# Performance work log

Hardware: AMD Instinct MI355X
Metric: run time of the kernel (lower is better)

## Reference

```python
import jax, jax.numpy as jnp
import numpy as np

DIM = 512
DEPTH = 6
HEADS = 8
HD = DIM // HEADS          # head dim = 64
HALF = HD // 4             # rope half_dim = 16
MLP_H = int(DIM * 4.0)
TOKENS = [1, 4, 16, 64]    # CLS, S1, S2, S3
N = sum(TOKENS)            # 85
MAX_FREQ = 10.0
BATCH = 1024
LN_EPS = 1e-5


def _build_mask():
    # CLS sees CLS+S3; each scale sees CLS+itself (block-diagonal + CLS column)
    m = np.full((N, N), -np.inf, dtype=np.float32)
    cum = np.cumsum([0] + TOKENS)  # [0,1,5,21,85]
    m[0, 0] = 0.0
    m[0, cum[3]:cum[4]] = 0.0
    for i in range(1, 4):
        s, e = cum[i], cum[i + 1]
        m[s:e, 0] = 0.0
        m[s:e, s:e] = 0.0
    return jnp.asarray(m)

MASK = _build_mask()
FREQS = jnp.exp(jnp.arange(HALF, dtype=jnp.float32) * (-np.log(MAX_FREQ) / HALF))


def _layer_norm(x, g, b):
    mu = x.mean(-1, keepdims=True)
    var = ((x - mu) ** 2).mean(-1, keepdims=True)
    return (x - mu) * jax.lax.rsqrt(var + LN_EPS) * g + b


def _rope2d(t, coords):
    # t: [B,H,P,HD], coords: [P,2] in [0,1]^2
    ang_x = coords[:, 0:1] * FREQS[None, :] * (2.0 * jnp.pi)  # [P,HALF]
    ang_y = coords[:, 1:2] * FREQS[None, :] * (2.0 * jnp.pi)
    cx, sx = jnp.cos(ang_x), jnp.sin(ang_x)
    cy, sy = jnp.cos(ang_y), jnp.sin(ang_y)
    B, H, P, _ = t.shape
    t = t.reshape(B, H, P, 4, HALF)
    x0, x1, x2, x3 = t[..., 0, :], t[..., 1, :], t[..., 2, :], t[..., 3, :]
    r = jnp.stack([x0 * cx - x1 * sx,
                   x0 * sx + x1 * cx,
                   x2 * cy - x3 * sy,
                   x2 * sy + x3 * cy], axis=3)
    return r.reshape(B, H, P, HD)


def _rope_skip_cls(t, coords):
    return jnp.concatenate([t[:, :, :1], _rope2d(t[:, :, 1:], coords)], axis=2)


def _block(x, coords, p):
    (ln1g, ln1b, qkvw, qkvb, projw, projb,
     ln2g, ln2b, f1w, f1b, f2w, f2b) = p
    B, Nn, D = x.shape
    h = _layer_norm(x, ln1g, ln1b)
    qkv = h @ qkvw + qkvb                         # [B,N,3D]
    qkv = qkv.reshape(B, Nn, 3, HEADS, HD).transpose(2, 0, 3, 1, 4)
    q, k, v = qkv[0], qkv[1], qkv[2]              # [B,H,N,HD]
    q = _rope_skip_cls(q, coords)
    k = _rope_skip_cls(k, coords)
    attn = jnp.einsum('bhqd,bhkd->bhqk', q, k) * (HD ** -0.5) + MASK
    attn = jax.nn.softmax(attn, axis=-1)
    out = jnp.einsum('bhqk,bhkd->bhqd', attn, v)
    out = out.transpose(0, 2, 1, 3).reshape(B, Nn, D)
    x = x + (out @ projw + projb)
    h = _layer_norm(x, ln2g, ln2b)
    h = jax.nn.gelu(h @ f1w + f1b, approximate=False) @ f2w + f2b
    return x + h


def setup_inputs() -> dict:
    key = jax.random.key(0)
    ks = jax.random.split(key, 8)
    s = 0.02
    nrm = lambda k, shape: jax.random.normal(k, shape, jnp.float32) * s
    return dict(
        x=jax.random.normal(ks[0], (BATCH, N, DIM), jnp.float32),
        coords=jax.random.uniform(ks[1], (N - 1, 2), jnp.float32),
        ln1_g=jnp.ones((DEPTH, DIM), jnp.float32),
        ln1_b=jnp.zeros((DEPTH, DIM), jnp.float32),
        qkv_w=nrm(ks[2], (DEPTH, DIM, 3 * DIM)),
        qkv_b=jnp.zeros((DEPTH, 3 * DIM), jnp.float32),
        proj_w=nrm(ks[3], (DEPTH, DIM, DIM)),
        proj_b=jnp.zeros((DEPTH, DIM), jnp.float32),
        ln2_g=jnp.ones((DEPTH, DIM), jnp.float32),
        ln2_b=jnp.zeros((DEPTH, DIM), jnp.float32),
        fc1_w=nrm(ks[4], (DEPTH, DIM, MLP_H)),
        fc1_b=jnp.zeros((DEPTH, MLP_H), jnp.float32),
        fc2_w=nrm(ks[5], (DEPTH, MLP_H, DIM)),
        fc2_b=jnp.zeros((DEPTH, DIM), jnp.float32),
    )


def reference(x, coords, ln1_g, ln1_b, qkv_w, qkv_b, proj_w, proj_b,
              ln2_g, ln2_b, fc1_w, fc1_b, fc2_w, fc2_b):
    for i in range(DEPTH):
        x = _block(x, coords,
                   (ln1_g[i], ln1_b[i], qkv_w[i], qkv_b[i], proj_w[i], proj_b[i],
                    ln2_g[i], ln2_b[i], fc1_w[i], fc1_b[i], fc2_w[i], fc2_b[i]))
    return x
```

## Files before the change

kernel.cpp:

```cpp
#include <hip/hip_runtime.h>
#include <hip/hip_bf16.h>
#include <math.h>

#define DIMX 512
#define NTOK 85
#define BATCH 1024
#define M_ROWS (BATCH * NTOK)
#define MLP_H 2048
#define DEPTH 6

typedef __attribute__((ext_vector_type(8))) short short8;
typedef __attribute__((ext_vector_type(4))) float f32x4;

__device__ inline float bf2f(ushort u) {
    union { unsigned int i; float f; } v; v.i = ((unsigned int)u) << 16; return v.f;
}
__device__ inline ushort f2bf(float f) {
    __hip_bfloat16 h = __float2bfloat16(f);
    union { __hip_bfloat16 h; ushort u; } v; v.h = h; return v.u;
}
__device__ inline unsigned int pack2(float a, float b) {
    return (unsigned int)f2bf(a) | ((unsigned int)f2bf(b) << 16);
}
__device__ inline float gelu_fast(float v) {
    float u = 1.5957691f * fmaf(0.044715f * v, v * v, v);
    return v / (1.0f + __expf(-u));
}

__device__ inline void gload16(const ushort* g, ushort* lds) {
    __builtin_amdgcn_global_load_lds(
        (const __attribute__((address_space(1))) unsigned int*)g,
        (__attribute__((address_space(3))) unsigned int*)lds, 16, 0, 0);
}

__global__ __launch_bounds__(256) void transpose_bf16(const float* __restrict__ in,
                                                      ushort* __restrict__ out,
                                                      int K, int N) {
    __shared__ float tile[32][33];
    int n0 = blockIdx.x * 32, k0 = blockIdx.y * 32;
    int tx = threadIdx.x, ty = threadIdx.y;
    #pragma unroll
    for (int j = 0; j < 32; j += 8)
        tile[ty + j][tx] = in[(size_t)(k0 + ty + j) * N + n0 + tx];
    __syncthreads();
    #pragma unroll
    for (int j = 0; j < 32; j += 8)
        out[(size_t)(n0 + ty + j) * K + k0 + tx] = f2bf(tile[tx][ty + j]);
}

__global__ void rope_table(const float* __restrict__ coords, float* __restrict__ tab) {
    int t = blockIdx.x;
    int idx = threadIdx.x;
    float freq = expf(-(float)idx * (2.302585093f / 16.0f));
    float twopi = 6.283185307179586f;
    float ax = coords[t * 2 + 0] * freq * twopi;
    float ay = coords[t * 2 + 1] * freq * twopi;
    tab[t * 64 + idx]      = cosf(ax);
    tab[t * 64 + 16 + idx] = sinf(ax);
    tab[t * 64 + 32 + idx] = cosf(ay);
    tab[t * 64 + 48 + idx] = sinf(ay);
}

__global__ __launch_bounds__(256) void ln_kernel(const float* __restrict__ x,
                                                 const float* __restrict__ g,
                                                 const float* __restrict__ bta,
                                                 ushort* __restrict__ out) {
    int w = threadIdx.x >> 6, lane = threadIdx.x & 63;
    size_t row = (size_t)blockIdx.x * 4 + w;
    const float* xr = x + row * DIMX;
    int c = lane * 8;
    float4 v0 = *(const float4*)(xr + c);
    float4 v1 = *(const float4*)(xr + c + 4);
    float s = v0.x + v0.y + v0.z + v0.w + v1.x + v1.y + v1.z + v1.w;
    #pragma unroll
    for (int m = 32; m; m >>= 1) s += __shfl_xor(s, m);
    float mu = s * (1.0f / 512.0f);
    float d0 = v0.x - mu, d1 = v0.y - mu, d2 = v0.z - mu, d3 = v0.w - mu;
    float d4 = v1.x - mu, d5 = v1.y - mu, d6 = v1.z - mu, d7 = v1.w - mu;
    float q = d0*d0 + d1*d1 + d2*d2 + d3*d3 + d4*d4 + d5*d5 + d6*d6 + d7*d7;
    #pragma unroll
    for (int m = 32; m; m >>= 1) q += __shfl_xor(q, m);
    float rs = rsqrtf(q * (1.0f / 512.0f) + 1e-5f);
    float4 g0 = *(const float4*)(g + c), g1 = *(const float4*)(g + c + 4);
    float4 b0 = *(const float4*)(bta + c), b1 = *(const float4*)(bta + c + 4);
    uint4 o;
    o.x = pack2(d0 * rs * g0.x + b0.x, d1 * rs * g0.y + b0.y);
    o.y = pack2(d2 * rs * g0.z + b0.z, d3 * rs * g0.w + b0.w);
    o.z = pack2(d4 * rs * g1.x + b1.x, d5 * rs * g1.y + b1.y);
    o.w = pack2(d6 * rs * g1.z + b1.z, d7 * rs * g1.w + b1.w);
    *(uint4*)&out[row * DIMX + c] = o;
}

template <int EPI>
__global__ __launch_bounds__(256, 2) void gemm_wide(const ushort* __restrict__ A,
                                                    const ushort* __restrict__ Bt,
                                                    const float* __restrict__ bias,
                                                    const float* __restrict__ inF,
                                                    float* __restrict__ outF,
                                                    ushort* __restrict__ outB,
                                                    int M, int N, int K,
                                                    const float* __restrict__ tab) {
    __shared__ ushort AsF[3 * 8192] __attribute__((aligned(16)));
    __shared__ ushort BsF[3 * 4096] __attribute__((aligned(16)));
    int tid = threadIdx.x;
    int w = tid >> 6, lane = tid & 63;
    int wm2 = (w >> 1) * 128;
    int wn = (w & 1) * 64;

    int nbx = gridDim.x;
    int nwg = nbx * gridDim.y;
    int orig = blockIdx.y * nbx + blockIdx.x;
    int q8 = nwg >> 3, r8 = nwg & 7;
    int xcd = orig & 7, loc = orig >> 3;
    int id = (xcd < r8) ? xcd * (q8 + 1) + loc : r8 * (q8 + 1) + (xcd - r8) * q8 + loc;
    int m0 = (id / nbx) * 256;
    int n0 = (id % nbx) * 128;

    int srow = tid >> 2;
    int scol = ((tid & 3) ^ ((srow >> 1) & 3)) * 8;
    int rA0 = m0 + srow;       if (rA0 >= M) rA0 = M - 1;
    int rA1 = m0 + 64 + srow;  if (rA1 >= M) rA1 = M - 1;
    int rA2 = m0 + 128 + srow; if (rA2 >= M) rA2 = M - 1;
    int rA3 = m0 + 192 + srow; if (rA3 >= M) rA3 = M - 1;
    const ushort* gA0 = A + (size_t)rA0 * K + scol;
    const ushort* gA1 = A + (size_t)rA1 * K + scol;
    const ushort* gA2 = A + (size_t)rA2 * K + scol;
    const ushort* gA3 = A + (size_t)rA3 * K + scol;
    const ushort* gB0 = Bt + (size_t)(n0 + srow) * K + scol;
    const ushort* gB1 = Bt + (size_t)(n0 + 64 + srow) * K + scol;
    int dwz = w * 512;
    int swA = 0, swB = 0;

#define STAGEW() do {                                                          \
        gload16(gA0, &AsF[swA + dwz]);                                         \
        gload16(gA1, &AsF[swA + 2048 + dwz]);                                  \
        gload16(gA2, &AsF[swA + 4096 + dwz]);                                  \
        gload16(gA3, &AsF[swA + 6144 + dwz]);                                  \
        gload16(gB0, &BsF[swB + dwz]);                                         \
        gload16(gB1, &BsF[swB + 2048 + dwz]);                                  \
        gA0 += 32; gA1 += 32; gA2 += 32; gA3 += 32; gB0 += 32; gB1 += 32;      \
        swA += 8192; if (swA == 24576) swA = 0;                                \
        swB += 4096; if (swB == 12288) swB = 0; } while (0)

    int l15 = lane & 15, lq = lane >> 4;
    int sw = (lq ^ ((l15 >> 1) & 3)) * 8;
    int aoff = (wm2 + l15) * 32 + sw;
    int boff = (wn + l15) * 32 + sw;
    int roffA = 0, roffB = 0;

    int NT = K >> 5;
    STAGEW(); STAGEW();

    f32x4 acc[8][4] = {};

    for (int t = 0; t < NT; ++t) {
        if (t < NT - 1) asm volatile("s_waitcnt vmcnt(6)" ::: "memory");
        else            asm volatile("s_waitcnt vmcnt(0)" ::: "memory");
        __builtin_amdgcn_s_barrier();
        short8 a[8], b[4];
        #pragma unroll
        for (int i = 0; i < 8; i++) a[i] = *(const short8*)&AsF[roffA + aoff + i * 512];
        #pragma unroll
        for (int j = 0; j < 4; j++) b[j] = *(const short8*)&BsF[roffB + boff + j * 512];
        if (t + 2 < NT) STAGEW();
        __builtin_amdgcn_s_setprio(1);
        #pragma unroll
        for (int i = 0; i < 8; i++)
            #pragma unroll
            for (int j = 0; j < 4; j++)
                acc[i][j] = __builtin_amdgcn_mfma_f32_16x16x32_bf16(a[i], b[j], acc[i][j], 0, 0, 0);
        __builtin_amdgcn_s_setprio(0);
        roffA += 8192; if (roffA == 24576) roffA = 0;
        roffB += 4096; if (roffB == 12288) roffB = 0;
    }
#undef STAGEW

    int cr = lq * 4;
    int cc = l15;
    if (EPI == 0) {
        bool ropeReg = (n0 + wn) < 1024;
        int gnb = n0 + wn + cc;
        float bb0 = bias[gnb], bb1 = bias[gnb + 16], bb2 = bias[gnb + 32], bb3 = bias[gnb + 48];
        #pragma unroll
        for (int i = 0; i < 8; i++) {
            #pragma unroll
            for (int rr = 0; rr < 4; rr++) {
                int gm = m0 + wm2 + i * 16 + cr + rr;
                if (gm >= M) continue;
                int n = gm % NTOK;
                float v0 = acc[i][0][rr] + bb0;
                float v1 = acc[i][1][rr] + bb1;
                float v2 = acc[i][2][rr] + bb2;
                float v3 = acc[i][3][rr] + bb3;
                if (ropeReg && n > 0) {
                    const float* tt = tab + (size_t)(n - 1) * 64 + cc;
                    float cx = tt[0], sx = tt[16], cy = tt[32], sy = tt[48];
                    float y0 = v0 * cx - v1 * sx;
                    float y1 = v0 * sx + v1 * cx;
                    float y2 = v2 * cy - v3 * sy;
                    float y3 = v2 * sy + v3 * cy;
                    v0 = y0; v1 = y1; v2 = y2; v3 = y3;
                }
                size_t o = (size_t)gm * N + gnb;
                outB[o]      = f2bf(v0);
                outB[o + 16] = f2bf(v1);
                outB[o + 32] = f2bf(v2);
                outB[o + 48] = f2bf(v3);
            }
        }
    } else {
        #pragma unroll
        for (int i = 0; i < 8; i++) {
            #pragma unroll
            for (int rr = 0; rr < 4; rr++) {
                int gm = m0 + wm2 + i * 16 + cr + rr;
                if (gm >= M) continue;
                #pragma unroll
                for (int j = 0; j < 4; j++) {
                    int gn = n0 + wn + j * 16 + cc;
                    float v = acc[i][j][rr] + bias[gn];
                    size_t o = (size_t)gm * N + gn;
                    if (EPI == 1) {
                        outF[o] = inF[o] + v;
                    } else {
                        outB[o] = f2bf(gelu_fast(v));
                    }
                }
            }
        }
    }
}

__global__ __launch_bounds__(256, 2) void gemm_nb(const ushort* __restrict__ A,
                                                  const ushort* __restrict__ Bt,
                                                  const float* __restrict__ bias,
                                                  ushort* __restrict__ outB,
                                                  int M, int N, int K) {
    __shared__ ushort LDS[4 * 10240] __attribute__((aligned(16)));
    int tid = threadIdx.x;
    int w = tid >> 6, lane = tid & 63;
    int wm = (w >> 1) * 96;
    int wn = (w & 1) * 64;

    int nbx = gridDim.x;
    int nwg = nbx * gridDim.y;
    int orig = blockIdx.y * nbx + blockIdx.x;
    int q8 = nwg >> 3, r8 = nwg & 7;
    int xcd = orig & 7, loc = orig >> 3;
    int id = (xcd < r8) ? xcd * (q8 + 1) + loc : r8 * (q8 + 1) + (xcd - r8) * q8 + loc;
    int m0 = (id / nbx) * 192;
    int n0 = (id % nbx) * 128;

    int srow = lane >> 2;
    int scol = ((lane & 3) ^ ((srow >> 1) & 3)) * 8;
    const ushort* pA[6];
    const ushort* pB[4];
    #pragma unroll
    for (int i = 0; i < 6; i++) {
        int r = m0 + wm + i * 16 + srow; if (r >= M) r = M - 1;
        pA[i] = A + (size_t)r * K + scol;
    }
    #pragma unroll
    for (int j = 0; j < 4; j++)
        pB[j] = Bt + (size_t)(n0 + wn + j * 16 + srow) * K + scol;

    ushort* LW = &LDS[w * 10240];

#define STAGE_NB(T) do { int kc = (T) * 32, s = ((T) & 1);                     \
        int da = s * 3072, db = 6144 + s * 2048;                               \
        gload16(pA[0] + kc, &LW[da]);                                          \
        gload16(pA[1] + kc, &LW[da + 512]);                                    \
        gload16(pA[2] + kc, &LW[da + 1024]);                                   \
        gload16(pA[3] + kc, &LW[da + 1536]);                                   \
        gload16(pA[4] + kc, &LW[da + 2048]);                                   \
        gload16(pA[5] + kc, &LW[da + 2560]);                                   \
        gload16(pB[0] + kc, &LW[db]);                                          \
        gload16(pB[1] + kc, &LW[db + 512]);                                    \
        gload16(pB[2] + kc, &LW[db + 1024]);                                   \
        gload16(pB[3] + kc, &LW[db + 1536]); } while (0)

    int l15 = lane & 15, lq = lane >> 4;
    int sw = (lq ^ ((l15 >> 1) & 3)) * 8;
    int foff = l15 * 32 + sw;

    int NT = K >> 5;
    STAGE_NB(0);

    f32x4 acc[6][4] = {};

    for (int t = 0; t < NT; ++t) {
        int ra = (t & 1) * 3072, rb = 6144 + (t & 1) * 2048;
        if (t + 1 < NT) {
            asm volatile("s_waitcnt lgkmcnt(0)" ::: "memory");
            STAGE_NB(t + 1);
            asm volatile("s_waitcnt vmcnt(10)" ::: "memory");
        } else {
            asm volatile("s_waitcnt vmcnt(0)" ::: "memory");
        }
        short8 a[6], b[4];
        #pragma unroll
        for (int i = 0; i < 6; i++) a[i] = *(const short8*)&LW[ra + foff + i * 512];
        #pragma unroll
        for (int j = 0; j < 4; j++) b[j] = *(const short8*)&LW[rb + foff + j * 512];
        __builtin_amdgcn_s_setprio(1);
        #pragma unroll
        for (int i = 0; i < 6; i++)
            #pragma unroll
            for (int j = 0; j < 4; j++)
                acc[i][j] = __builtin_amdgcn_mfma_f32_16x16x32_bf16(a[i], b[j], acc[i][j], 0, 0, 0);
        __builtin_amdgcn_s_setprio(0);
    }
#undef STAGE_NB

    int cr = lq * 4;
    int cc = l15;
    #pragma unroll
    for (int i = 0; i < 6; i++) {
        #pragma unroll
        for (int rr = 0; rr < 4; rr++) {
            int gm = m0 + wm + i * 16 + cr + rr;
            if (gm >= M) continue;
            #pragma unroll
            for (int j = 0; j < 4; j++) {
                int gn = n0 + wn + j * 16 + cc;
                float v = acc[i][j][rr] + bias[gn];
                outB[(size_t)gm * N + gn] = f2bf(gelu_fast(v));
            }
        }
    }
}

__global__ __launch_bounds__(384) void attn_kernel(const ushort* __restrict__ qkv,
                                                   ushort* __restrict__ out) {
    __shared__ ushort SU[13824] __attribute__((aligned(16)));
    __shared__ ushort Vt[6656]  __attribute__((aligned(16)));
    int bh = blockIdx.x;
    int b = bh >> 3, h = bh & 7;
    int tid = threadIdx.x;
    size_t base = (size_t)b * NTOK * 1536 + h * 64;

    for (int it = tid; it < 1536; it += 384) {
        int mat = (it >= 768) ? 1 : 0;
        int item = it - mat * 768;
        int n = item >> 3, g = item & 7;
        short8 v = {};
        if (n < NTOK)
            v = *(const short8*)&qkv[base + (size_t)n * 1536 + mat * 512 + g * 8];
        *(short8*)&SU[mat * 6912 + n * 72 + g * 8] = v;
    }
    for (int it = tid; it < 768; it += 384) {
        int n = it % 96;
        int d0 = (it / 96) * 8;
        short8 v = {};
        if (n < NTOK)
            v = *(const short8*)&qkv[base + (size_t)n * 1536 + 1024 + d0];
        #pragma unroll
        for (int j = 0; j < 8; j++)
            Vt[(d0 + j) * 104 + n] = (ushort)v[j];
    }
    __syncthreads();

    int wid = tid >> 6;
    int lane = tid & 63;
    int q = lane >> 4, c = lane & 15;
    int i0 = wid * 16;

    f32x4 acc[6] = {};
    #pragma unroll
    for (int kk = 0; kk < 2; kk++) {
        short8 aq = *(const short8*)&SU[(i0 + c) * 72 + kk * 32 + q * 8];
        #pragma unroll
        for (int t = 0; t < 6; t++) {
            short8 bk = *(const short8*)&SU[6912 + (t * 16 + c) * 72 + kk * 32 + q * 8];
            acc[t] = __builtin_amdgcn_mfma_f32_16x16x32_bf16(aq, bk, acc[t], 0, 0, 0);
        }
    }
    __syncthreads();

    #pragma unroll
    for (int r = 0; r < 4; r++) {
        int i = i0 + q * 4 + r;
        int si = (i == 0) ? 3 : (i < 5 ? 1 : (i < 21 ? 2 : 3));
        float vs[6];
        float m = -1e30f;
        #pragma unroll
        for (int t = 0; t < 6; t++) {
            int j = t * 16 + c;
            int sj = (j == 0) ? si : (j < 5 ? 1 : (j < 21 ? 2 : (j < NTOK ? 3 : -1)));
            float v = (sj == si) ? acc[t][r] * 0.125f : -1e30f;
            vs[t] = v;
            m = fmaxf(m, v);
        }
        #pragma unroll
        for (int mk = 8; mk; mk >>= 1) m = fmaxf(m, __shfl_xor(m, mk));
        float s = 0.f, ps[6];
        #pragma unroll
        for (int t = 0; t < 6; t++) { ps[t] = __expf(vs[t] - m); s += ps[t]; }
        #pragma unroll
        for (int mk = 8; mk; mk >>= 1) s += __shfl_xor(s, mk);
        float inv = 1.0f / s;
        #pragma unroll
        for (int t = 0; t < 6; t++)
            SU[i * 104 + t * 16 + c] = f2bf(ps[t] * inv);
    }
    __syncthreads();

    f32x4 o2[4] = {};
    #pragma unroll
    for (int kk = 0; kk < 3; kk++) {
        short8 ap = *(const short8*)&SU[(i0 + c) * 104 + kk * 32 + q * 8];
        #pragma unroll
        for (int nt = 0; nt < 4; nt++) {
            short8 bv = *(const short8*)&Vt[(nt * 16 + c) * 104 + kk * 32 + q * 8];
            o2[nt] = __builtin_amdgcn_mfma_f32_16x16x32_bf16(ap, bv, o2[nt], 0, 0, 0);
        }
    }
    size_t orow = (size_t)b * NTOK;
    #pragma unroll
    for (int nt = 0; nt < 4; nt++) {
        #pragma unroll
        for (int r = 0; r < 4; r++) {
            int i = i0 + q * 4 + r;
            if (i < NTOK)
                out[(orow + i) * DIMX + h * 64 + nt * 16 + c] = f2bf(o2[nt][r]);
        }
    }
}

extern "C" void kernel_launch(void* const* d_in, const int* in_sizes, int n_in,
                              void* d_out, int out_size, void* d_ws, size_t ws_size,
                              hipStream_t stream) {
    const float* x_in    = (const float*)d_in[0];
    const float* coords  = (const float*)d_in[1];
    const float* ln1_g   = (const float*)d_in[2];
    const float* ln1_b   = (const float*)d_in[3];
    const float* qkv_w   = (const float*)d_in[4];
    const float* qkv_b   = (const float*)d_in[5];
    const float* proj_w  = (const float*)d_in[6];
    const float* proj_b  = (const float*)d_in[7];
    const float* ln2_g   = (const float*)d_in[8];
    const float* ln2_b   = (const float*)d_in[9];
    const float* fc1_w   = (const float*)d_in[10];
    const float* fc1_b   = (const float*)d_in[11];
    const float* fc2_w   = (const float*)d_in[12];
    const float* fc2_b   = (const float*)d_in[13];

    char* ws = (char*)d_ws;
    size_t off = 0;
    auto alloc = [&](size_t bytes) -> void* {
        void* p = ws + off;
        off += (bytes + 255) & ~(size_t)255;
        return p;
    };
    auto asz = [](size_t b) { return (b + 255) & ~(size_t)255; };

    const size_t WPL = 512 * 1536 + 512 * 512 + 512 * 2048 + 2048 * 512;

    size_t fixed = asz(WPL * DEPTH * sizeof(ushort)) + asz(84 * 64 * sizeof(float));
    int Bc = 1024;
    while (Bc > 4) {
        size_t rc = (size_t)Bc * NTOK;
        size_t need = fixed + asz(rc * DIMX * sizeof(ushort)) + asz(rc * MLP_H * sizeof(ushort));
        if (need <= ws_size) break;
        Bc >>= 1;
    }
    size_t Rc = (size_t)Bc * NTOK;

    ushort* wt   = (ushort*)alloc(WPL * DEPTH * sizeof(ushort));
    float*  tab  = (float*)alloc(84 * 64 * sizeof(float));
    ushort* hbuf = (ushort*)alloc(Rc * DIMX * sizeof(ushort));
    ushort* big  = (ushort*)alloc(Rc * MLP_H * sizeof(ushort));

    rope_table<<<84, 16, 0, stream>>>(coords, tab);

    dim3 tb(32, 8);
    for (int l = 0; l < DEPTH; l++) {
        ushort* wl = wt + (size_t)l * WPL;
        transpose_bf16<<<dim3(1536 / 32, 512 / 32), tb, 0, stream>>>(
            qkv_w + (size_t)l * 512 * 1536, wl, 512, 1536);
        transpose_bf16<<<dim3(512 / 32, 512 / 32), tb, 0, stream>>>(
            proj_w + (size_t)l * 512 * 512, wl + 786432, 512, 512);
        transpose_bf16<<<dim3(2048 / 32, 512 / 32), tb, 0, stream>>>(
            fc1_w + (size_t)l * 512 * 2048, wl + 1048576, 512, 2048);
        transpose_bf16<<<dim3(512 / 32, 2048 / 32), tb, 0, stream>>>(
            fc2_w + (size_t)l * 2048 * 512, wl + 2097152, 2048, 512);
    }

    int mt256 = (int)(Rc / 256);
    int mt192 = (int)((Rc + 191) / 192);
    int lnblocks = (int)(Rc / 4);
    for (int c = 0; c < BATCH / Bc; c++) {
        float* xc = (float*)d_out + (size_t)c * Rc * DIMX;
        const float* xin_c = x_in + (size_t)c * Rc * DIMX;
        int Mc = (int)Rc;
        for (int l = 0; l < DEPTH; l++) {
            ushort* wl = wt + (size_t)l * WPL;
            const float* xsrc = (l == 0) ? xin_c : xc;
            ln_kernel<<<lnblocks, 256, 0, stream>>>(
                xsrc, ln1_g + l * 512, ln1_b + l * 512, hbuf);
            gemm_wide<0><<<dim3(1536 / 128, mt256), 256, 0, stream>>>(
                hbuf, wl, qkv_b + (size_t)l * 1536, nullptr, nullptr, big,
                Mc, 1536, 512, tab);
            attn_kernel<<<Bc * 8, 384, 0, stream>>>(big, hbuf);
            gemm_wide<1><<<dim3(512 / 128, mt256), 256, 0, stream>>>(
                hbuf, wl + 786432, proj_b + (size_t)l * 512, xsrc, xc, nullptr,
                Mc, 512, 512, nullptr);
            ln_kernel<<<lnblocks, 256, 0, stream>>>(
                xc, ln2_g + l * 512, ln2_b + l * 512, hbuf);
            gemm_nb<<<dim3(2048 / 128, mt192), 256, 0, stream>>>(
                hbuf, wl + 1048576, fc1_b + (size_t)l * 2048, big,
                Mc, 2048, 512);
            gemm_wide<1><<<dim3(512 / 128, mt256), 256, 0, stream>>>(
                big, wl + 2097152, fc2_b + (size_t)l * 512, xc, xc, nullptr,
                Mc, 512, 2048, nullptr);
        }
    }
}
```

Measured before the change: 7.209 ms.

## Replace per-wave fc1 GEMM with shared-LDS 512-thread triple-buffered kernel

The fc1 GEMM moves from a 256-thread kernel, where each wave staged its own private A/B tiles (192x128 block), to a 512-thread kernel with a 256x128 block tile. The eight waves share A/B tiles in LDS through a three-stage ring buffer with barrier synchronisation. This removes redundant global loads of shared operand rows and gives deeper prefetch. It adds block-wide barriers, fewer accumulators per wave, and a templated epilogue that also carries an unused RoPE path for the qkv GEMM.

```diff
diff --git a/kernel.cpp b/kernel.cpp
--- a/kernel.cpp
+++ b/kernel.cpp
@@ -231,15 +231,20 @@
     }
 }
 
-__global__ __launch_bounds__(256, 2) void gemm_nb(const ushort* __restrict__ A,
-                                                  const ushort* __restrict__ Bt,
-                                                  const float* __restrict__ bias,
-                                                  ushort* __restrict__ outB,
-                                                  int M, int N, int K) {
-    __shared__ ushort LDS[4 * 10240] __attribute__((aligned(16)));
+template <int EPI>
+__global__ __launch_bounds__(512, 4) void gemm_e(const ushort* __restrict__ A,
+                                                 const ushort* __restrict__ Bt,
+                                                 const float* __restrict__ bias,
+                                                 const float* __restrict__ inF,
+                                                 float* __restrict__ outF,
+                                                 ushort* __restrict__ outB,
+                                                 int M, int N, int K,
+                                                 const float* __restrict__ tab) {
+    __shared__ ushort AsF[3 * 8192] __attribute__((aligned(16)));
+    __shared__ ushort BsF[3 * 4096] __attribute__((aligned(16)));
     int tid = threadIdx.x;
     int w = tid >> 6, lane = tid & 63;
-    int wm = (w >> 1) * 96;
+    int wm = (w >> 1) * 64;
     int wn = (w & 1) * 64;
 
     int nbx = gridDim.x;
@@ -248,83 +253,111 @@
     int q8 = nwg >> 3, r8 = nwg & 7;
     int xcd = orig & 7, loc = orig >> 3;
     int id = (xcd < r8) ? xcd * (q8 + 1) + loc : r8 * (q8 + 1) + (xcd - r8) * q8 + loc;
-    int m0 = (id / nbx) * 192;
+    int m0 = (id / nbx) * 256;
     int n0 = (id % nbx) * 128;
 
-    int srow = lane >> 2;
-    int scol = ((lane & 3) ^ ((srow >> 1) & 3)) * 8;
-    const ushort* pA[6];
-    const ushort* pB[4];
-    #pragma unroll
-    for (int i = 0; i < 6; i++) {
-        int r = m0 + wm + i * 16 + srow; if (r >= M) r = M - 1;
-        pA[i] = A + (size_t)r * K + scol;
-    }
-    #pragma unroll
-    for (int j = 0; j < 4; j++)
-        pB[j] = Bt + (size_t)(n0 + wn + j * 16 + srow) * K + scol;
-
-    ushort* LW = &LDS[w * 10240];
-
-#define STAGE_NB(T) do { int kc = (T) * 32, s = ((T) & 1);                     \
-        int da = s * 3072, db = 6144 + s * 2048;                               \
-        gload16(pA[0] + kc, &LW[da]);                                          \
-        gload16(pA[1] + kc, &LW[da + 512]);                                    \
-        gload16(pA[2] + kc, &LW[da + 1024]);                                   \
-        gload16(pA[3] + kc, &LW[da + 1536]);                                   \
-        gload16(pA[4] + kc, &LW[da + 2048]);                                   \
-        gload16(pA[5] + kc, &LW[da + 2560]);                                   \
-        gload16(pB[0] + kc, &LW[db]);                                          \
-        gload16(pB[1] + kc, &LW[db + 512]);                                    \
-        gload16(pB[2] + kc, &LW[db + 1024]);                                   \
-        gload16(pB[3] + kc, &LW[db + 1536]); } while (0)
+    int srow = tid >> 2;
+    int scol = ((tid & 3) ^ ((srow >> 1) & 3)) * 8;
+    int rA0 = m0 + srow;        if (rA0 >= M) rA0 = M - 1;
+    int rA1 = m0 + 128 + srow;  if (rA1 >= M) rA1 = M - 1;
+    const ushort* gA0 = A + (size_t)rA0 * K + scol;
+    const ushort* gA1 = A + (size_t)rA1 * K + scol;
+    const ushort* gB0 = Bt + (size_t)(n0 + srow) * K + scol;
+    int dwz = w * 512;
+    int swA = 0, swB = 0;
+
+#define STAGEE() do {                                                          \
+        gload16(gA0, &AsF[swA + dwz]);                                         \
+        gload16(gA1, &AsF[swA + 4096 + dwz]);                                  \
+        gload16(gB0, &BsF[swB + dwz]);                                         \
+        gA0 += 32; gA1 += 32; gB0 += 32;                                       \
+        swA += 8192; if (swA == 24576) swA = 0;                                \
+        swB += 4096; if (swB == 12288) swB = 0; } while (0)
 
     int l15 = lane & 15, lq = lane >> 4;
     int sw = (lq ^ ((l15 >> 1) & 3)) * 8;
-    int foff = l15 * 32 + sw;
+    int aoff = (wm + l15) * 32 + sw;
+    int boff = (wn + l15) * 32 + sw;
+    int roffA = 0, roffB = 0;
 
     int NT = K >> 5;
-    STAGE_NB(0);
-
-    f32x4 acc[6][4] = {};
+    STAGEE(); STAGEE();
+
+    f32x4 acc[4][4] = {};
 
     for (int t = 0; t < NT; ++t) {
-        int ra = (t & 1) * 3072, rb = 6144 + (t & 1) * 2048;
-        if (t + 1 < NT) {
-            asm volatile("s_waitcnt lgkmcnt(0)" ::: "memory");
-            STAGE_NB(t + 1);
-            asm volatile("s_waitcnt vmcnt(10)" ::: "memory");
-        } else {
-            asm volatile("s_waitcnt vmcnt(0)" ::: "memory");
-        }
-        short8 a[6], b[4];
-        #pragma unroll
-        for (int i = 0; i < 6; i++) a[i] = *(const short8*)&LW[ra + foff + i * 512];
-        #pragma unroll
-        for (int j = 0; j < 4; j++) b[j] = *(const short8*)&LW[rb + foff + j * 512];
+        if (t < NT - 1) asm volatile("s_waitcnt vmcnt(3)" ::: "memory");
+        else            asm volatile("s_waitcnt vmcnt(0)" ::: "memory");
+        __builtin_amdgcn_s_barrier();
+        short8 a[4], b[4];
+        #pragma unroll
+        for (int i = 0; i < 4; i++) a[i] = *(const short8*)&AsF[roffA + aoff + i * 512];
+        #pragma unroll
+        for (int j = 0; j < 4; j++) b[j] = *(const short8*)&BsF[roffB + boff + j * 512];
+        if (t + 2 < NT) STAGEE();
         __builtin_amdgcn_s_setprio(1);
         #pragma unroll
-        for (int i = 0; i < 6; i++)
+        for (int i = 0; i < 4; i++)
             #pragma unroll
             for (int j = 0; j < 4; j++)
                 acc[i][j] = __builtin_amdgcn_mfma_f32_16x16x32_bf16(a[i], b[j], acc[i][j], 0, 0, 0);
         __builtin_amdgcn_s_setprio(0);
-    }
-#undef STAGE_NB
+        roffA += 8192; if (roffA == 24576) roffA = 0;
+        roffB += 4096; if (roffB == 12288) roffB = 0;
+    }
+#undef STAGEE
 
     int cr = lq * 4;
     int cc = l15;
-    #pragma unroll
-    for (int i = 0; i < 6; i++) {
-        #pragma unroll
-        for (int rr = 0; rr < 4; rr++) {
-            int gm = m0 + wm + i * 16 + cr + rr;
-            if (gm >= M) continue;
+    if (EPI == 0) {
+        bool ropeReg = (n0 + wn) < 1024;
+        int gnb = n0 + wn + cc;
+        float bb0 = bias[gnb], bb1 = bias[gnb + 16], bb2 = bias[gnb + 32], bb3 = bias[gnb + 48];
+        #pragma unroll
+        for (int i = 0; i < 4; i++) {
             #pragma unroll
-            for (int j = 0; j < 4; j++) {
-                int gn = n0 + wn + j * 16 + cc;
-                float v = acc[i][j][rr] + bias[gn];
-                outB[(size_t)gm * N + gn] = f2bf(gelu_fast(v));
+            for (int rr = 0; rr < 4; rr++) {
+                int gm = m0 + wm + i * 16 + cr + rr;
+                if (gm >= M) continue;
+                int n = gm % NTOK;
+                float v0 = acc[i][0][rr] + bb0;
+                float v1 = acc[i][1][rr] + bb1;
+                float v2 = acc[i][2][rr] + bb2;
+                float v3 = acc[i][3][rr] + bb3;
+                if (ropeReg && n > 0) {
+                    const float* tt = tab + (size_t)(n - 1) * 64 + cc;
+                    float cx = tt[0], sx = tt[16], cy = tt[32], sy = tt[48];
+                    float y0 = v0 * cx - v1 * sx;
+                    float y1 = v0 * sx + v1 * cx;
+                    float y2 = v2 * cy - v3 * sy;
+                    float y3 = v2 * sy + v3 * cy;
+                    v0 = y0; v1 = y1; v2 = y2; v3 = y3;
+                }
+                size_t o = (size_t)gm * N + gnb;
+                outB[o]      = f2bf(v0);
+                outB[o + 16] = f2bf(v1);
+                outB[o + 32] = f2bf(v2);
+                outB[o + 48] = f2bf(v3);
+            }
+        }
+    } else {
+        #pragma unroll
+        for (int i = 0; i < 4; i++) {
+            #pragma unroll
+            for (int rr = 0; rr < 4; rr++) {
+                int gm = m0 + wm + i * 16 + cr + rr;
+                if (gm >= M) continue;
+                #pragma unroll
+                for (int j = 0; j < 4; j++) {
+                    int gn = n0 + wn + j * 16 + cc;
+                    float v = acc[i][j][rr] + bias[gn];
+                    size_t o = (size_t)gm * N + gn;
+                    if (EPI == 1) {
+                        outF[o] = inF[o] + v;
+                    } else {
+                        outB[o] = f2bf(gelu_fast(v));
+                    }
+                }
             }
         }
     }
@@ -487,7 +520,6 @@
     }
 
     int mt256 = (int)(Rc / 256);
-    int mt192 = (int)((Rc + 191) / 192);
     int lnblocks = (int)(Rc / 4);
     for (int c = 0; c < BATCH / Bc; c++) {
         float* xc = (float*)d_out + (size_t)c * Rc * DIMX;
@@ -507,9 +539,9 @@
                 Mc, 512, 512, nullptr);
             ln_kernel<<<lnblocks, 256, 0, stream>>>(
                 xc, ln2_g + l * 512, ln2_b + l * 512, hbuf);
-            gemm_nb<<<dim3(2048 / 128, mt192), 256, 0, stream>>>(
-                hbuf, wl + 1048576, fc1_b + (size_t)l * 2048, big,
-                Mc, 2048, 512);
+            gemm_e<2><<<dim3(2048 / 128, mt256), 512, 0, stream>>>(
+                hbuf, wl + 1048576, fc1_b + (size_t)l * 2048, nullptr, nullptr,
+                big, Mc, 2048, 512, nullptr);
             gemm_wide<1><<<dim3(512 / 128, mt256), 256, 0, stream>>>(
                 big, wl + 2097152, fc2_b + (size_t)l * 512, xc, xc, nullptr,
                 Mc, 512, 2048, nullptr);
```

Result: faster. 6.812 ms (-5.5%).
